# Performance work log

Hardware: AMD Instinct MI355X
Metric: run time of the kernel (lower is better)

## Reference

```python
import jax, jax.numpy as jnp
import numpy as np

B, S, HID = 1, 4096, 2048
H, KV, D = 16, 8, 128
EPS = 1e-6
ROPE_THETA = 10000.0


def _rms_norm(x, w, eps=EPS):
    # x: [..., D], normalize over last dim in fp32 like Qwen3 RMSNorm
    xf = x.astype(jnp.float32)
    var = jnp.mean(xf * xf, axis=-1, keepdims=True)
    return (xf * jax.lax.rsqrt(var + eps)).astype(x.dtype) * w


def _rotate_half(x):
    x1, x2 = jnp.split(x, 2, axis=-1)
    return jnp.concatenate([-x2, x1], axis=-1)


def setup_inputs() -> dict:
    key = jax.random.key(0)
    ks = jax.random.split(key, 6)
    hidden_states = jax.random.normal(ks[0], (B, S, HID), dtype=jnp.float32)
    wq = jax.random.normal(ks[1], (H * D, HID), dtype=jnp.float32) * 0.02
    wk = jax.random.normal(ks[2], (KV * D, HID), dtype=jnp.float32) * 0.02
    wv = jax.random.normal(ks[3], (KV * D, HID), dtype=jnp.float32) * 0.02
    wo = jax.random.normal(ks[4], (HID, H * D), dtype=jnp.float32) * 0.02
    q_norm_w = jnp.ones((D,), dtype=jnp.float32)
    k_norm_w = jnp.ones((D,), dtype=jnp.float32)
    # real rotary tables: inv_freq over half dim, duplicated (HF convention)
    inv_freq = 1.0 / (ROPE_THETA ** (jnp.arange(0, D, 2, dtype=jnp.float32) / D))
    pos = jnp.arange(S, dtype=jnp.float32)
    freqs = pos[:, None] * inv_freq[None, :]          # [S, D/2]
    emb = jnp.concatenate([freqs, freqs], axis=-1)    # [S, D]
    cos = jnp.cos(emb)[None].astype(jnp.float32)      # [B, S, D]
    sin = jnp.sin(emb)[None].astype(jnp.float32)
    return {"hidden_states": hidden_states, "cos": cos, "sin": sin,
            "wq": wq, "wk": wk, "wv": wv, "wo": wo,
            "q_norm_w": q_norm_w, "k_norm_w": k_norm_w}


def reference(hidden_states, cos, sin, wq, wk, wv, wo, q_norm_w, k_norm_w):
    b, s, _ = hidden_states.shape
    scaling = D ** -0.5
    # QKV projections (no bias), reshape to heads, QK RMSNorm, then [b, h, s, d]
    q = _rms_norm(jnp.einsum('bsh,oh->bso', hidden_states, wq).reshape(b, s, H, D), q_norm_w)
    k = _rms_norm(jnp.einsum('bsh,oh->bso', hidden_states, wk).reshape(b, s, KV, D), k_norm_w)
    v = jnp.einsum('bsh,oh->bso', hidden_states, wv).reshape(b, s, KV, D)
    q = q.transpose(0, 2, 1, 3)  # [b, H, s, d]
    k = k.transpose(0, 2, 1, 3)  # [b, KV, s, d]
    v = v.transpose(0, 2, 1, 3)
    # RoPE (cos/sin broadcast over head dim)
    c = cos[:, None, :, :]
    sn = sin[:, None, :, :]
    q = q * c + _rotate_half(q) * sn
    k = k * c + _rotate_half(k) * sn
    # GQA: repeat KV heads to H
    groups = H // KV
    k = jnp.repeat(k, groups, axis=1)
    v = jnp.repeat(v, groups, axis=1)
    # eager causal attention, softmax in fp32
    scores = jnp.einsum('bhqd,bhkd->bhqk', q, k) * scaling
    causal = jnp.tril(jnp.ones((s, s), dtype=bool))
    scores = jnp.where(causal[None, None], scores, jnp.finfo(jnp.float32).min)
    attn = jax.nn.softmax(scores.astype(jnp.float32), axis=-1).astype(q.dtype)
    out = jnp.einsum('bhqk,bhkd->bhqd', attn, v)
    out = out.transpose(0, 2, 1, 3).reshape(b, s, H * D)
    return jnp.einsum('bso,ho->bsh', out, wo)
```

## Files before the change

### kernel.cpp

```cpp
#include <hip/hip_runtime.h>
#include <hip/hip_bf16.h>

typedef __hip_bfloat16 bf16;
typedef __attribute__((ext_vector_type(8))) short short8;
typedef __attribute__((ext_vector_type(4))) float f32x4;

#define S_LEN 4096
#define HID_DIM 2048

#define QSCALE ((float)(0.08838834764831845 * 1.4426950408889634))

__device__ __forceinline__ void gld_lds16(const void* g, void* l) {
  __builtin_amdgcn_global_load_lds(
      (const __attribute__((address_space(1))) void*)g,
      (__attribute__((address_space(3))) void*)l, 16, 0, 0);
}

__device__ __forceinline__ float fexp2(float x) {
  return __builtin_amdgcn_exp2f(x);
}

__device__ __forceinline__ unsigned cvtpk_bf16(float lo, float hi) {
  unsigned r;
  asm("v_cvt_pk_bf16_f32 %0, %1, %2" : "=v"(r) : "v"(lo), "v"(hi));
  return r;
}

__global__ __launch_bounds__(256) void k_cvt4(
    const float* __restrict__ hs, const float* __restrict__ wq,
    const float* __restrict__ wk, const float* __restrict__ wv,
    bf16* __restrict__ Ah, bf16* __restrict__ Wqkv) {
  long u = (long)blockIdx.x * 256 + threadIdx.x;
  const float* src;
  bf16* dst;
  if (u < 1048576) {
    src = hs; dst = Ah;
  } else if (u < 1572864) {
    u -= 1048576; src = wq; dst = Wqkv;
  } else if (u < 1835008) {
    u -= 1572864; src = wk; dst = Wqkv + (long)2048 * 2048;
  } else {
    u -= 1835008; src = wv; dst = Wqkv + (long)3072 * 2048;
  }
  const long i = u * 8;
  float4 a = *reinterpret_cast<const float4*>(src + i);
  float4 b = *reinterpret_cast<const float4*>(src + i + 4);
  float v[8] = {a.x, a.y, a.z, a.w, b.x, b.y, b.z, b.w};
  short8 o;
#pragma unroll
  for (int j = 0; j < 8; ++j) {
    bf16 h = __float2bfloat16(v[j]);
    o[j] = *reinterpret_cast<short*>(&h);
  }
  *reinterpret_cast<short8*>(dst + i) = o;
}

__device__ __forceinline__ int2 xcd_swz(int nx) {
  const int bid = blockIdx.y * nx + blockIdx.x;
  const int nwg = nx * gridDim.y;
  const int q = nwg >> 3;
  const int swz = (bid & 7) * q + (bid >> 3);
  return make_int2(swz % nx, swz / nx);
}

template <typename OutT>
__global__ __launch_bounds__(512, 1) void k_gemm256(
    const bf16* __restrict__ A, const bf16* __restrict__ B,
    OutT* __restrict__ C, int M, int N, int K) {
  __shared__ bf16 Al[2][256 * 64];
  __shared__ bf16 Bl[2][256 * 64];
  const int tid = threadIdx.x;
  const int lane = tid & 63;
  const int wid = tid >> 6;
  const int wr = wid >> 2;
  const int wc = wid & 3;
  const int2 bxy = xcd_swz(gridDim.x);
  const long brow = (long)bxy.y * 256;
  const long bcol = (long)bxy.x * 256;
  const int NT = K >> 6;

  auto stage = [&](int kt, int buf) {
    const bf16* At = A + brow * K + kt * 64;
    const bf16* Bt = B + bcol * K + kt * 64;
#pragma unroll
    for (int i = 0; i < 4; ++i) {
      const int ch = tid + i * 512;
      const int row = ch >> 3;
      const int j = (ch & 7) ^ (row & 7);
      gld_lds16(At + (size_t)row * K + j * 8, &Al[buf][(wid * 64 + i * 512) * 8]);
    }
#pragma unroll
    for (int i = 0; i < 4; ++i) {
      const int ch = tid + i * 512;
      const int row = ch >> 3;
      const int j = (ch & 7) ^ (row & 7);
      gld_lds16(Bt + (size_t)row * K + j * 8, &Bl[buf][(wid * 64 + i * 512) * 8]);
    }
  };

  f32x4 acc0[4][4], acc1[4][4];
#pragma unroll
  for (int m = 0; m < 4; ++m)
#pragma unroll
    for (int n = 0; n < 4; ++n) {
      acc0[m][n] = (f32x4){0.f, 0.f, 0.f, 0.f};
      acc1[m][n] = (f32x4){0.f, 0.f, 0.f, 0.f};
    }

  const int l15 = lane & 15;
  const int cp0 = ((lane >> 4) ^ (lane & 7)) * 8;
  const int cp1 = ((4 + (lane >> 4)) ^ (lane & 7)) * 8;

  stage(0, 0);
  stage(1, 1);
  asm volatile("s_waitcnt vmcnt(8)" ::: "memory");
  __builtin_amdgcn_s_barrier();

  for (int kt = 0; kt < NT; ++kt) {
    const bf16* Ab = &Al[kt & 1][0];
    const bf16* Bb = &Bl[kt & 1][0];
    short8 bB[4][2], aA[4][2];
#pragma unroll
    for (int n = 0; n < 4; ++n) {
      const int rb = (wc * 64 + n * 16 + l15) * 64;
      bB[n][0] = *reinterpret_cast<const short8*>(&Bb[rb + cp0]);
      bB[n][1] = *reinterpret_cast<const short8*>(&Bb[rb + cp1]);
    }
#pragma unroll
    for (int m = 0; m < 4; ++m) {
      const int ra = (wr * 128 + m * 16 + l15) * 64;
      aA[m][0] = *reinterpret_cast<const short8*>(&Ab[ra + cp0]);
      aA[m][1] = *reinterpret_cast<const short8*>(&Ab[ra + cp1]);
    }
    __builtin_amdgcn_s_setprio(1);
#pragma unroll
    for (int m = 0; m < 4; ++m)
#pragma unroll
      for (int n = 0; n < 4; ++n) {
        acc0[m][n] = __builtin_amdgcn_mfma_f32_16x16x32_bf16(aA[m][0], bB[n][0],
                                                             acc0[m][n], 0, 0, 0);
        acc0[m][n] = __builtin_amdgcn_mfma_f32_16x16x32_bf16(aA[m][1], bB[n][1],
                                                             acc0[m][n], 0, 0, 0);
      }
    __builtin_amdgcn_s_setprio(0);
#pragma unroll
    for (int m = 0; m < 4; ++m) {
      const int ra = (wr * 128 + 64 + m * 16 + l15) * 64;
      aA[m][0] = *reinterpret_cast<const short8*>(&Ab[ra + cp0]);
      aA[m][1] = *reinterpret_cast<const short8*>(&Ab[ra + cp1]);
    }
    __builtin_amdgcn_s_setprio(1);
#pragma unroll
    for (int m = 0; m < 4; ++m)
#pragma unroll
      for (int n = 0; n < 4; ++n) {
        acc1[m][n] = __builtin_amdgcn_mfma_f32_16x16x32_bf16(aA[m][0], bB[n][0],
                                                             acc1[m][n], 0, 0, 0);
        acc1[m][n] = __builtin_amdgcn_mfma_f32_16x16x32_bf16(aA[m][1], bB[n][1],
                                                             acc1[m][n], 0, 0, 0);
      }
    __builtin_amdgcn_s_setprio(0);

    if (kt + 1 < NT) {
      __builtin_amdgcn_s_barrier();
      if (kt + 2 < NT) {
        stage(kt + 2, kt & 1);
        asm volatile("s_waitcnt vmcnt(8)" ::: "memory");
      } else {
        asm volatile("s_waitcnt vmcnt(0)" ::: "memory");
      }
      __builtin_amdgcn_s_barrier();
    }
  }

#pragma unroll
  for (int mh = 0; mh < 2; ++mh) {
#pragma unroll
    for (int m = 0; m < 4; ++m) {
      const long r0 = brow + wr * 128 + mh * 64 + m * 16 + (lane >> 4) * 4;
#pragma unroll
      for (int n = 0; n < 4; ++n) {
        const long c0 = bcol + wc * 64 + n * 16 + l15;
        const f32x4 v = mh ? acc1[m][n] : acc0[m][n];
#pragma unroll
        for (int r = 0; r < 4; ++r) {
          if constexpr (sizeof(OutT) == 2)
            C[(r0 + r) * N + c0] = __float2bfloat16(v[r]);
          else
            C[(r0 + r) * N + c0] = v[r];
        }
      }
    }
  }
}

__global__ __launch_bounds__(512, 1) void k_gemm_op(
    const bf16* __restrict__ A, const bf16* __restrict__ B,
    float* __restrict__ C, int M, int N, int K) {
  __shared__ bf16 Al[2][256 * 64];
  __shared__ bf16 Bl[2][128 * 64];
  const int tid = threadIdx.x;
  const int lane = tid & 63;
  const int wid = tid >> 6;
  const int wr = wid >> 1;
  const int wc = wid & 1;
  const int2 bxy = xcd_swz(gridDim.x);
  const long brow = (long)bxy.y * 256;
  const long bcol = (long)bxy.x * 128;
  const int NT = K >> 6;

  auto stage = [&](int kt, int buf) {
    const bf16* At = A + brow * K + kt * 64;
    const bf16* Bt = B + bcol * K + kt * 64;
#pragma unroll
    for (int i = 0; i < 4; ++i) {
      const int ch = tid + i * 512;
      const int row = ch >> 3;
      const int j = (ch & 7) ^ (row & 7);
      gld_lds16(At + (size_t)row * K + j * 8, &Al[buf][(wid * 64 + i * 512) * 8]);
    }
#pragma unroll
    for (int i = 0; i < 2; ++i) {
      const int ch = tid + i * 512;
      const int row = ch >> 3;
      const int j = (ch & 7) ^ (row & 7);
      gld_lds16(Bt + (size_t)row * K + j * 8, &Bl[buf][(wid * 64 + i * 512) * 8]);
    }
  };

  f32x4 acc[4][4];
#pragma unroll
  for (int m = 0; m < 4; ++m)
#pragma unroll
    for (int n = 0; n < 4; ++n) acc[m][n] = (f32x4){0.f, 0.f, 0.f, 0.f};

  const int l15 = lane & 15;
  const int cp0 = ((lane >> 4) ^ (lane & 7)) * 8;
  const int cp1 = ((4 + (lane >> 4)) ^ (lane & 7)) * 8;

  stage(0, 0);
  stage(1, 1);
  asm volatile("s_waitcnt vmcnt(6)" ::: "memory");
  __builtin_amdgcn_s_barrier();

  for (int kt = 0; kt < NT; ++kt) {
    const bf16* Ab = &Al[kt & 1][0];
    const bf16* Bb = &Bl[kt & 1][0];
    short8 bB[4][2], aA[4][2];
#pragma unroll
    for (int n = 0; n < 4; ++n) {
      const int rb = (wc * 64 + n * 16 + l15) * 64;
      bB[n][0] = *reinterpret_cast<const short8*>(&Bb[rb + cp0]);
      bB[n][1] = *reinterpret_cast<const short8*>(&Bb[rb + cp1]);
    }
#pragma unroll
    for (int m = 0; m < 4; ++m) {
      const int ra = (wr * 64 + m * 16 + l15) * 64;
      aA[m][0] = *reinterpret_cast<const short8*>(&Ab[ra + cp0]);
      aA[m][1] = *reinterpret_cast<const short8*>(&Ab[ra + cp1]);
    }
    __builtin_amdgcn_s_setprio(1);
#pragma unroll
    for (int m = 0; m < 4; ++m)
#pragma unroll
      for (int n = 0; n < 4; ++n) {
        acc[m][n] = __builtin_amdgcn_mfma_f32_16x16x32_bf16(aA[m][0], bB[n][0],
                                                            acc[m][n], 0, 0, 0);
        acc[m][n] = __builtin_amdgcn_mfma_f32_16x16x32_bf16(aA[m][1], bB[n][1],
                                                            acc[m][n], 0, 0, 0);
      }
    __builtin_amdgcn_s_setprio(0);

    if (kt + 1 < NT) {
      __builtin_amdgcn_s_barrier();
      if (kt + 2 < NT) {
        stage(kt + 2, kt & 1);
        asm volatile("s_waitcnt vmcnt(6)" ::: "memory");
      } else {
        asm volatile("s_waitcnt vmcnt(0)" ::: "memory");
      }
      __builtin_amdgcn_s_barrier();
    }
  }

#pragma unroll
  for (int m = 0; m < 4; ++m) {
    const long r0 = brow + wr * 64 + m * 16 + (lane >> 4) * 4;
#pragma unroll
    for (int n = 0; n < 4; ++n) {
      const long c0 = bcol + wc * 64 + n * 16 + l15;
#pragma unroll
      for (int r = 0; r < 4; ++r) C[(r0 + r) * N + c0] = acc[m][n][r];
    }
  }
}

__global__ __launch_bounds__(256) void k_prep(
    const bf16* __restrict__ QKVb, const float* __restrict__ cosb,
    const float* __restrict__ sinb, const float* __restrict__ qw,
    const float* __restrict__ kw, const float* __restrict__ wo,
    bf16* __restrict__ Qb, bf16* __restrict__ Kb, bf16* __restrict__ Vt,
    bf16* __restrict__ Wo) {
  __shared__ bf16 Lds[64][136];
  const int tid = threadIdx.x;
  if (blockIdx.x < 24576) {
    const int lane = tid & 63;
    const int u = blockIdx.x * 4 + (tid >> 6);
    const int s = u / 24;
    const int idx = u - s * 24;
    const bf16* src = QKVb + (size_t)s * 4096 + idx * 128;
    float x0 = __bfloat162float(src[lane]);
    float x1 = __bfloat162float(src[lane + 64]);
    float ss = x0 * x0 + x1 * x1;
#pragma unroll
    for (int off = 1; off < 64; off <<= 1) ss += __shfl_xor(ss, off);
    const float rn = rsqrtf(ss * (1.f / 128.f) + 1e-6f);
    const float* w = (idx < 16) ? qw : kw;
    x0 = x0 * rn * w[lane];
    x1 = x1 * rn * w[lane + 64];
    const float c0 = cosb[(size_t)s * 128 + lane];
    const float c1 = cosb[(size_t)s * 128 + lane + 64];
    const float s0 = sinb[(size_t)s * 128 + lane];
    const float s1 = sinb[(size_t)s * 128 + lane + 64];
    float o0 = x0 * c0 - x1 * s0;
    float o1 = x1 * c1 + x0 * s1;
    if (idx < 16) { o0 *= QSCALE; o1 *= QSCALE; }
    bf16* dst = (idx < 16) ? (Qb + ((size_t)idx * S_LEN + s) * 128)
                           : (Kb + ((size_t)(idx - 16) * S_LEN + s) * 128);
    dst[lane] = __float2bfloat16(o0);
    dst[lane + 64] = __float2bfloat16(o1);
  } else if (blockIdx.x < 25088) {
    const int b = blockIdx.x - 24576;
    const int s0 = (b & 63) * 64;
    const int kv = b >> 6;
#pragma unroll
    for (int pass = 0; pass < 4; ++pass) {
      const int c = tid + pass * 256;
      const int r = c >> 4;
      const int off = (c & 15) * 8;
      *reinterpret_cast<short8*>(&Lds[r][off]) =
          *reinterpret_cast<const short8*>(
              &QKVb[(size_t)(s0 + r) * 4096 + 3072 + kv * 128 + off]);
    }
    __syncthreads();
#pragma unroll
    for (int pass = 0; pass < 4; ++pass) {
      const int c = tid + pass * 256;
      const int d = c >> 3;
      const int so = (c & 7) * 8;
      short8 o;
#pragma unroll
      for (int j = 0; j < 8; ++j) {
        bf16 e = Lds[so + j][d];
        o[j] = *reinterpret_cast<short*>(&e);
      }
      *reinterpret_cast<short8*>(&Vt[((size_t)kv * 128 + d) * S_LEN + s0 + so]) =
          o;
    }
  } else {
    const long u = (long)(blockIdx.x - 25088) * 256 + tid;
    const long i = u * 8;
    float4 a = *reinterpret_cast<const float4*>(wo + i);
    float4 b = *reinterpret_cast<const float4*>(wo + i + 4);
    float v[8] = {a.x, a.y, a.z, a.w, b.x, b.y, b.z, b.w};
    short8 o;
#pragma unroll
    for (int j = 0; j < 8; ++j) {
      bf16 h = __float2bfloat16(v[j]);
      o[j] = *reinterpret_cast<short*>(&h);
    }
    *reinterpret_cast<short8*>(Wo + i) = o;
  }
}

__global__ __launch_bounds__(256) void k_attn(const bf16* __restrict__ Qb,
                                              const bf16* __restrict__ Kb,
                                              const bf16* __restrict__ Vt_g,
                                              bf16* __restrict__ AO) {
  __shared__ bf16 Kl[2][64 * 128];
  __shared__ bf16 Vl[2][128 * 64];
  __shared__ bf16 Pl[4][16 * 64];
  const int tid = threadIdx.x;
  const int lane = tid & 63;
  const int wv = tid >> 6;
  const int lin = blockIdx.y * 32 + blockIdx.x;
  const int xcd = lin & 7;
  const int jj = lin >> 3;
  const int h = 2 * xcd + (jj & 1);
  const int bx = jj >> 1;
  const int kvh = h >> 1;
  const int c16 = lane & 15;
  const int hi = lane >> 4;
  const int kk = hi * 8;

  const bf16* Kbase = Kb + (size_t)kvh * S_LEN * 128;
  const bf16* Vbase = Vt_g + (size_t)kvh * 128 * S_LEN;

  auto stage = [&](int t, int buf) {
    const bf16* Kt = Kbase + (size_t)t * 64 * 128;
    const bf16* Vt = Vbase + t * 64;
#pragma unroll
    for (int p = 0; p < 4; ++p) {
      const int ch = tid + p * 256;
      const int row = ch >> 4, cp = ch & 15;
      const int c = (cp & 8) | ((cp & 7) ^ (row & 7));
      gld_lds16(Kt + row * 128 + c * 8, &Kl[buf][(wv * 64 + p * 256) * 8]);
    }
#pragma unroll
    for (int p = 0; p < 4; ++p) {
      const int ch = tid + p * 256;
      const int d = ch >> 3, cp = ch & 7;
      const int c = cp ^ (d & 7);
      gld_lds16(Vt + (size_t)d * S_LEN + c * 8, &Vl[buf][(wv * 64 + p * 256) * 8]);
    }
  };

  for (int half = 0; half < 2; ++half) {
    const int qt = half ? (63 - bx) : bx;
    const int qrow = qt * 64 + wv * 16;
    const int grow = qrow + c16;

    __syncthreads();
    stage(0, 0);

    short8 qf[4];
    {
      const bf16* qp = Qb + ((size_t)h * S_LEN + grow) * 128 + kk;
#pragma unroll
      for (int ks = 0; ks < 4; ++ks)
        qf[ks] = *reinterpret_cast<const short8*>(qp + ks * 32);
    }

    f32x4 oacc[8];
#pragma unroll
    for (int i = 0; i < 8; ++i) oacc[i] = (f32x4){0.f, 0.f, 0.f, 0.f};
    float m_run = -1e30f;
    float l_part = 0.f;

    auto tile = [&](int t, int buf, bool mask) {
      f32x4 sacc[4];
#pragma unroll
      for (int nt = 0; nt < 4; ++nt) sacc[nt] = (f32x4){0.f, 0.f, 0.f, 0.f};
      __builtin_amdgcn_s_setprio(1);
#pragma unroll
      for (int ks = 0; ks < 4; ++ks) {
#pragma unroll
        for (int nt = 0; nt < 4; ++nt) {
          const int row = nt * 16 + c16;
          const int ck = ks * 4 + hi;
          const int ckp = (ck & 8) | ((ck & 7) ^ (row & 7));
          short8 kf =
              *reinterpret_cast<const short8*>(&Kl[buf][row * 128 + ckp * 8]);
          sacc[nt] = __builtin_amdgcn_mfma_f32_16x16x32_bf16(kf, qf[ks],
                                                             sacc[nt], 0, 0, 0);
        }
      }
      __builtin_amdgcn_s_setprio(0);

      float tm = -1e30f;
#pragma unroll
      for (int nt = 0; nt < 4; ++nt)
#pragma unroll
        for (int r = 0; r < 4; ++r) {
          float sv = sacc[nt][r];
          if (mask && (t * 64 + nt * 16 + 4 * hi + r > grow)) sv = -1e30f;
          sacc[nt][r] = sv;
          tm = fmaxf(tm, sv);
        }
      tm = fmaxf(tm, __shfl_xor(tm, 16));
      tm = fmaxf(tm, __shfl_xor(tm, 32));
      if (__any(tm > m_run + 8.f)) {
        const float mn = fmaxf(m_run, tm);
        const float alpha = fexp2(m_run - mn);
        m_run = mn;
        l_part *= alpha;
#pragma unroll
        for (int dn = 0; dn < 8; ++dn) oacc[dn] *= alpha;
      }

#pragma unroll
      for (int nt = 0; nt < 4; ++nt) {
        const float p0 = fexp2(sacc[nt][0] - m_run);
        const float p1 = fexp2(sacc[nt][1] - m_run);
        const float p2 = fexp2(sacc[nt][2] - m_run);
        const float p3 = fexp2(sacc[nt][3] - m_run);
        l_part += (p0 + p1) + (p2 + p3);
        uint2 w2;
        w2.x = cvtpk_bf16(p0, p1);
        w2.y = cvtpk_bf16(p2, p3);
        const int chunk = (2 * nt + (hi >> 1)) ^ (c16 & 7);
        const int base = c16 * 64 + chunk * 8 + 4 * (hi & 1);
        *reinterpret_cast<uint2*>(&Pl[wv][base]) = w2;
      }

      __builtin_amdgcn_s_setprio(1);
#pragma unroll
      for (int ks = 0; ks < 2; ++ks) {
        const int pc = (ks * 4 + hi) ^ (c16 & 7);
        short8 pf =
            *reinterpret_cast<const short8*>(&Pl[wv][c16 * 64 + pc * 8]);
#pragma unroll
        for (int dn = 0; dn < 8; ++dn) {
          const int d = dn * 16 + c16;
          const int cvp = (ks * 4 + hi) ^ (d & 7);
          short8 vf =
              *reinterpret_cast<const short8*>(&Vl[buf][d * 64 + cvp * 8]);
          oacc[dn] =
              __builtin_amdgcn_mfma_f32_16x16x32_bf16(vf, pf, oacc[dn], 0, 0, 0);
        }
      }
      __builtin_amdgcn_s_setprio(0);
    };

    __syncthreads();
    int cur = 0;
    for (int t = 0; t < qt; ++t) {
      stage(t + 1, cur ^ 1);
      tile(t, cur, false);
      __syncthreads();
      cur ^= 1;
    }
    tile(qt, cur, true);

    float lt = l_part;
    lt += __shfl_xor(lt, 16);
    lt += __shfl_xor(lt, 32);
    const float inv = 1.f / lt;
    bf16* dst = AO + (size_t)grow * HID_DIM + h * 128;
#pragma unroll
    for (int dn = 0; dn < 8; ++dn) {
#pragma unroll
      for (int w = 0; w < 2; ++w) {
        const unsigned pk = cvtpk_bf16(oacc[dn][2 * w] * inv,
                                       oacc[dn][2 * w + 1] * inv);
        *reinterpret_cast<unsigned*>(&dst[dn * 16 + 4 * hi + 2 * w]) = pk;
      }
    }
  }
}

extern "C" void kernel_launch(void* const* d_in, const int* in_sizes, int n_in,
                              void* d_out, int out_size, void* d_ws,
                              size_t ws_size, hipStream_t stream) {
  (void)in_sizes; (void)n_in; (void)out_size; (void)ws_size;
  const float* hs = (const float*)d_in[0];
  const float* cosb = (const float*)d_in[1];
  const float* sinb = (const float*)d_in[2];
  const float* wq = (const float*)d_in[3];
  const float* wk = (const float*)d_in[4];
  const float* wv = (const float*)d_in[5];
  const float* wo = (const float*)d_in[6];
  const float* qnw = (const float*)d_in[7];
  const float* knw = (const float*)d_in[8];
  float* out = (float*)d_out;
  char* ws = (char*)d_ws;

  bf16* Ah = (bf16*)(ws + 0);
  bf16* Wqkv = (bf16*)(ws + 16777216);
  bf16* Wo = (bf16*)(ws + 33554432);
  bf16* QKVb = (bf16*)(ws + 41943040);
  bf16* Qb = (bf16*)(ws + 75497472);
  bf16* Kb = (bf16*)(ws + 92274688);
  bf16* AO = (bf16*)(ws + 109051904);
  bf16* Vt = (bf16*)(ws + 125829120);

  k_cvt4<<<dim3(8192), dim3(256), 0, stream>>>(hs, wq, wk, wv, Ah, Wqkv);
  k_gemm256<bf16><<<dim3(16, 16), dim3(512), 0, stream>>>(Ah, Wqkv, QKVb, 4096,
                                                          4096, 2048);
  k_prep<<<dim3(27136), dim3(256), 0, stream>>>(QKVb, cosb, sinb, qnw, knw, wo,
                                                Qb, Kb, Vt, Wo);
  k_attn<<<dim3(32, 16), dim3(256), 0, stream>>>(Qb, Kb, Vt, AO);
  k_gemm_op<<<dim3(16, 16), dim3(512), 0, stream>>>(AO, Wo, out, 4096, 2048,
                                                    2048);
}
```

Baseline: 253.4 us.

## Process paired causal query tiles in one KV sweep sharing K/V loads

Result: slower. 394.8 us (+55.8%).

```diff
diff --git a/kernel.cpp b/kernel.cpp
--- a/kernel.cpp
+++ b/kernel.cpp
@@ -387,8 +387,11 @@
   const int xcd = lin & 7;
   const int jj = lin >> 3;
   const int h = 2 * xcd + (jj & 1);
-  const int bx = jj >> 1;
-  const int kvh = h >> 1;
+  const int u = jj >> 1;
+  const int bx = (u < 16) ? u : (47 - u);
+  const int kvh = xcd;
+  const int qlo = bx;
+  const int NT = 64 - bx;
   const int c16 = lane & 15;
   const int hi = lane >> 4;
   const int kk = hi * 8;
@@ -415,76 +418,91 @@
     }
   };
 
-  for (int half = 0; half < 2; ++half) {
-    const int qt = half ? (63 - bx) : bx;
-    const int qrow = qt * 64 + wv * 16;
-    const int grow = qrow + c16;
-
-    __syncthreads();
-    stage(0, 0);
-
-    short8 qf[4];
-    {
-      const bf16* qp = Qb + ((size_t)h * S_LEN + grow) * 128 + kk;
-#pragma unroll
-      for (int ks = 0; ks < 4; ++ks)
-        qf[ks] = *reinterpret_cast<const short8*>(qp + ks * 32);
-    }
-
-    f32x4 oacc[8];
-#pragma unroll
-    for (int i = 0; i < 8; ++i) oacc[i] = (f32x4){0.f, 0.f, 0.f, 0.f};
-    float m_run = -1e30f;
-    float l_part = 0.f;
-
-    auto tile = [&](int t, int buf, bool mask) {
-      f32x4 sacc[4];
-#pragma unroll
-      for (int nt = 0; nt < 4; ++nt) sacc[nt] = (f32x4){0.f, 0.f, 0.f, 0.f};
-      __builtin_amdgcn_s_setprio(1);
-#pragma unroll
-      for (int ks = 0; ks < 4; ++ks) {
-#pragma unroll
-        for (int nt = 0; nt < 4; ++nt) {
-          const int row = nt * 16 + c16;
-          const int ck = ks * 4 + hi;
-          const int ckp = (ck & 8) | ((ck & 7) ^ (row & 7));
-          short8 kf =
-              *reinterpret_cast<const short8*>(&Kl[buf][row * 128 + ckp * 8]);
-          sacc[nt] = __builtin_amdgcn_mfma_f32_16x16x32_bf16(kf, qf[ks],
-                                                             sacc[nt], 0, 0, 0);
-        }
-      }
-      __builtin_amdgcn_s_setprio(0);
-
+  const int growA = qlo * 64 + wv * 16 + c16;
+  const int growB = (63 - bx) * 64 + wv * 16 + c16;
+
+  short8 qfA[4], qfB[4];
+  {
+    const bf16* qpA = Qb + ((size_t)h * S_LEN + growA) * 128 + kk;
+    const bf16* qpB = Qb + ((size_t)h * S_LEN + growB) * 128 + kk;
+#pragma unroll
+    for (int ks = 0; ks < 4; ++ks) {
+      qfA[ks] = *reinterpret_cast<const short8*>(qpA + ks * 32);
+      qfB[ks] = *reinterpret_cast<const short8*>(qpB + ks * 32);
+    }
+  }
+
+  f32x4 oA[8], oB[8];
+#pragma unroll
+  for (int i = 0; i < 8; ++i) {
+    oA[i] = (f32x4){0.f, 0.f, 0.f, 0.f};
+    oB[i] = (f32x4){0.f, 0.f, 0.f, 0.f};
+  }
+  float mA = -1e30f, mB = -1e30f, lA = 0.f, lB = 0.f;
+
+  stage(0, 0);
+  __syncthreads();
+
+  int cur = 0;
+  for (int t = 0; t < NT; ++t) {
+    if (t + 1 < NT) stage(t + 1, cur ^ 1);
+    const bool activeA = (t <= qlo);
+    const bool maskA = (t == qlo);
+    const bool maskB = (t == NT - 1);
+
+    f32x4 sA[4], sB[4];
+#pragma unroll
+    for (int nt = 0; nt < 4; ++nt) {
+      sA[nt] = (f32x4){0.f, 0.f, 0.f, 0.f};
+      sB[nt] = (f32x4){0.f, 0.f, 0.f, 0.f};
+    }
+    __builtin_amdgcn_s_setprio(1);
+#pragma unroll
+    for (int ks = 0; ks < 4; ++ks) {
+#pragma unroll
+      for (int nt = 0; nt < 4; ++nt) {
+        const int row = nt * 16 + c16;
+        const int ck = ks * 4 + hi;
+        const int ckp = (ck & 8) | ((ck & 7) ^ (row & 7));
+        short8 kf =
+            *reinterpret_cast<const short8*>(&Kl[cur][row * 128 + ckp * 8]);
+        if (activeA)
+          sA[nt] = __builtin_amdgcn_mfma_f32_16x16x32_bf16(kf, qfA[ks], sA[nt],
+                                                           0, 0, 0);
+        sB[nt] = __builtin_amdgcn_mfma_f32_16x16x32_bf16(kf, qfB[ks], sB[nt],
+                                                         0, 0, 0);
+      }
+    }
+    __builtin_amdgcn_s_setprio(0);
+
+    if (activeA) {
       float tm = -1e30f;
 #pragma unroll
       for (int nt = 0; nt < 4; ++nt)
 #pragma unroll
         for (int r = 0; r < 4; ++r) {
-          float sv = sacc[nt][r];
-          if (mask && (t * 64 + nt * 16 + 4 * hi + r > grow)) sv = -1e30f;
-          sacc[nt][r] = sv;
+          float sv = sA[nt][r];
+          if (maskA && (t * 64 + nt * 16 + 4 * hi + r > growA)) sv = -1e30f;
+          sA[nt][r] = sv;
           tm = fmaxf(tm, sv);
         }
       tm = fmaxf(tm, __shfl_xor(tm, 16));
       tm = fmaxf(tm, __shfl_xor(tm, 32));
-      if (__any(tm > m_run + 8.f)) {
-        const float mn = fmaxf(m_run, tm);
-        const float alpha = fexp2(m_run - mn);
-        m_run = mn;
-        l_part *= alpha;
-#pragma unroll
-        for (int dn = 0; dn < 8; ++dn) oacc[dn] *= alpha;
-      }
-
+      if (__any(tm > mA + 8.f)) {
+        const float mn = fmaxf(mA, tm);
+        const float alpha = fexp2(mA - mn);
+        mA = mn;
+        lA *= alpha;
+#pragma unroll
+        for (int dn = 0; dn < 8; ++dn) oA[dn] *= alpha;
+      }
 #pragma unroll
       for (int nt = 0; nt < 4; ++nt) {
-        const float p0 = fexp2(sacc[nt][0] - m_run);
-        const float p1 = fexp2(sacc[nt][1] - m_run);
-        const float p2 = fexp2(sacc[nt][2] - m_run);
-        const float p3 = fexp2(sacc[nt][3] - m_run);
-        l_part += (p0 + p1) + (p2 + p3);
+        const float p0 = fexp2(sA[nt][0] - mA);
+        const float p1 = fexp2(sA[nt][1] - mA);
+        const float p2 = fexp2(sA[nt][2] - mA);
+        const float p3 = fexp2(sA[nt][3] - mA);
+        lA += (p0 + p1) + (p2 + p3);
         uint2 w2;
         w2.x = cvtpk_bf16(p0, p1);
         w2.y = cvtpk_bf16(p2, p3);
@@ -492,7 +510,6 @@
         const int base = c16 * 64 + chunk * 8 + 4 * (hi & 1);
         *reinterpret_cast<uint2*>(&Pl[wv][base]) = w2;
       }
-
       __builtin_amdgcn_s_setprio(1);
 #pragma unroll
       for (int ks = 0; ks < 2; ++ks) {
@@ -504,38 +521,103 @@
           const int d = dn * 16 + c16;
           const int cvp = (ks * 4 + hi) ^ (d & 7);
           short8 vf =
-              *reinterpret_cast<const short8*>(&Vl[buf][d * 64 + cvp * 8]);
-          oacc[dn] =
-              __builtin_amdgcn_mfma_f32_16x16x32_bf16(vf, pf, oacc[dn], 0, 0, 0);
+              *reinterpret_cast<const short8*>(&Vl[cur][d * 64 + cvp * 8]);
+          oA[dn] = __builtin_amdgcn_mfma_f32_16x16x32_bf16(vf, pf, oA[dn],
+                                                           0, 0, 0);
         }
       }
       __builtin_amdgcn_s_setprio(0);
-    };
-
-    __syncthreads();
-    int cur = 0;
-    for (int t = 0; t < qt; ++t) {
-      stage(t + 1, cur ^ 1);
-      tile(t, cur, false);
+    }
+
+    {
+      float tm = -1e30f;
+#pragma unroll
+      for (int nt = 0; nt < 4; ++nt)
+#pragma unroll
+        for (int r = 0; r < 4; ++r) {
+          float sv = sB[nt][r];
+          if (maskB && (t * 64 + nt * 16 + 4 * hi + r > growB)) sv = -1e30f;
+          sB[nt][r] = sv;
+          tm = fmaxf(tm, sv);
+        }
+      tm = fmaxf(tm, __shfl_xor(tm, 16));
+      tm = fmaxf(tm, __shfl_xor(tm, 32));
+      if (__any(tm > mB + 8.f)) {
+        const float mn = fmaxf(mB, tm);
+        const float alpha = fexp2(mB - mn);
+        mB = mn;
+        lB *= alpha;
+#pragma unroll
+        for (int dn = 0; dn < 8; ++dn) oB[dn] *= alpha;
+      }
+#pragma unroll
+      for (int nt = 0; nt < 4; ++nt) {
+        const float p0 = fexp2(sB[nt][0] - mB);
+        const float p1 = fexp2(sB[nt][1] - mB);
+        const float p2 = fexp2(sB[nt][2] - mB);
+        const float p3 = fexp2(sB[nt][3] - mB);
+        lB += (p0 + p1) + (p2 + p3);
+        uint2 w2;
+        w2.x = cvtpk_bf16(p0, p1);
+        w2.y = cvtpk_bf16(p2, p3);
+        const int chunk = (2 * nt + (hi >> 1)) ^ (c16 & 7);
+        const int base = c16 * 64 + chunk * 8 + 4 * (hi & 1);
+        *reinterpret_cast<uint2*>(&Pl[wv][base]) = w2;
+      }
+      __builtin_amdgcn_s_setprio(1);
+#pragma unroll
+      for (int ks = 0; ks < 2; ++ks) {
+        const int pc = (ks * 4 + hi) ^ (c16 & 7);
+        short8 pf =
+            *reinterpret_cast<const short8*>(&Pl[wv][c16 * 64 + pc * 8]);
+#pragma unroll
+        for (int dn = 0; dn < 8; ++dn) {
+          const int d = dn * 16 + c16;
+          const int cvp = (ks * 4 + hi) ^ (d & 7);
+          short8 vf =
+              *reinterpret_cast<const short8*>(&Vl[cur][d * 64 + cvp * 8]);
+          oB[dn] = __builtin_amdgcn_mfma_f32_16x16x32_bf16(vf, pf, oB[dn],
+                                                           0, 0, 0);
+        }
+      }
+      __builtin_amdgcn_s_setprio(0);
+    }
+
+    if (t + 1 < NT) {
       __syncthreads();
       cur ^= 1;
     }
-    tile(qt, cur, true);
-
-    float lt = l_part;
+  }
+
+  {
+    float lt = lA;
     lt += __shfl_xor(lt, 16);
     lt += __shfl_xor(lt, 32);
     const float inv = 1.f / lt;
-    bf16* dst = AO + (size_t)grow * HID_DIM + h * 128;
-#pragma unroll
-    for (int dn = 0; dn < 8; ++dn) {
+    bf16* dst = AO + (size_t)growA * HID_DIM + h * 128;
+#pragma unroll
+    for (int dn = 0; dn < 8; ++dn)
 #pragma unroll
       for (int w = 0; w < 2; ++w) {
-        const unsigned pk = cvtpk_bf16(oacc[dn][2 * w] * inv,
-                                       oacc[dn][2 * w + 1] * inv);
+        const unsigned pk =
+            cvtpk_bf16(oA[dn][2 * w] * inv, oA[dn][2 * w + 1] * inv);
         *reinterpret_cast<unsigned*>(&dst[dn * 16 + 4 * hi + 2 * w]) = pk;
       }
-    }
+  }
+  {
+    float lt = lB;
+    lt += __shfl_xor(lt, 16);
+    lt += __shfl_xor(lt, 32);
+    const float inv = 1.f / lt;
+    bf16* dst = AO + (size_t)growB * HID_DIM + h * 128;
+#pragma unroll
+    for (int dn = 0; dn < 8; ++dn)
+#pragma unroll
+      for (int w = 0; w < 2; ++w) {
+        const unsigned pk =
+            cvtpk_bf16(oB[dn][2 * w] * inv, oB[dn][2 * w + 1] * inv);
+        *reinterpret_cast<unsigned*>(&dst[dn * 16 + 4 * hi + 2 * w]) = pk;
+      }
   }
 }
 
```
